# Optimization experiments

Hardware: AMD Instinct MI355X
Metric: run time of the kernel (lower is better)

## Reference

```python
import jax, jax.numpy as jnp
import numpy as np

N_HEAD = 16
HEAD_SIZE = 1024
EMBED = 1024
MULTI_HEAD_SIZE = HEAD_SIZE // N_HEAD  # 64; used only as the softmax scale (source bug)
B, S = 4, 2048


def setup_inputs() -> dict:
    key = jax.random.key(0)
    k1, k2, k3, k4 = jax.random.split(key, 4)
    x = jax.random.normal(k1, (B, S, EMBED), dtype=jnp.float32)
    w_qkv = jax.random.normal(k2, (3 * HEAD_SIZE, EMBED), dtype=jnp.float32) * 0.02
    w_proj = jax.random.normal(k3, (EMBED, HEAD_SIZE), dtype=jnp.float32) * 0.02
    b_proj = jax.random.normal(k4, (EMBED,), dtype=jnp.float32) * 0.02
    return {"x": x, "w_qkv": w_qkv, "w_proj": w_proj, "b_proj": b_proj}


def reference(x, w_qkv, w_proj, b_proj):
    # Fused QKV projection (Linear, no bias): [B,S,E] @ [E,3H] -> split
    qkv = jnp.einsum("bse,he->bsh", x, w_qkv)  # [B,S,3H]
    q, k, v = jnp.split(qkv, 3, axis=-1)       # each [B,S,H]
    # Source's non-flash path: attention over FULL Head_size dim (not per-head),
    # scaled by sqrt(multi_head_size) -- reproduced faithfully.
    scale = 1.0 / np.sqrt(MULTI_HEAD_SIZE).astype(np.float32)
    scores = jnp.einsum("bqh,bkh->bqk", q, k) * scale  # [B,S,S]
    probs = jax.nn.softmax(scores, axis=-1)            # dropout = identity (eval)
    out = jnp.einsum("bqk,bkh->bqh", probs, v)         # [B,S,H]
    # Faithful scrambling reshape: transpose(1,2).contiguous().view(B,S,H)
    Bn, Sn, H = out.shape
    out = jnp.swapaxes(out, 1, 2).reshape(Bn, Sn, H)
    # Output projection + residual dropout (identity in eval)
    out = jnp.einsum("bsh,eh->bse", out, w_proj) + b_proj
    return out
```

## Files before the change

### kernel.cpp

```cpp
#include <hip/hip_runtime.h>


typedef float f32x4 __attribute__((ext_vector_type(4)));
typedef short bf16x8 __attribute__((ext_vector_type(8)));
typedef short bf16x4 __attribute__((ext_vector_type(4)));
typedef unsigned short u16;

__device__ inline u16 f2bf(float f) {
  union { float f; unsigned u; } x; x.f = f;
  unsigned r = x.u + 0x7fffu + ((x.u >> 16) & 1u);
  return (u16)(r >> 16);
}

__device__ inline void gload_lds16(const void* g, void* l) {
  __builtin_amdgcn_global_load_lds(
      (const __attribute__((address_space(1))) void*)g,
      (__attribute__((address_space(3))) void*)l, 16, 0, 0);
}

__global__ __launch_bounds__(256) void cvt_kernel(const float* __restrict__ in,
                                                  u16* __restrict__ out, int n8) {
  int i = blockIdx.x * 256 + threadIdx.x;
  if (i >= n8) return;
  f32x4 a = *(const f32x4*)&in[(long)i * 8];
  f32x4 b = *(const f32x4*)&in[(long)i * 8 + 4];
  bf16x8 o;
#pragma unroll
  for (int j = 0; j < 4; ++j) { o[j] = (short)f2bf(a[j]); o[4 + j] = (short)f2bf(b[j]); }
  *(bf16x8*)&out[(long)i * 8] = o;
}

__global__ __launch_bounds__(256) void transpose_v(const u16* __restrict__ qkvb,
                                                   u16* __restrict__ vT) {
  __shared__ u16 tile[64][72];
  const int t = threadIdx.x;
  const long b = blockIdx.z;
  const int k0 = blockIdx.x * 64, h0 = blockIdx.y * 64;
  const u16* v = qkvb + b * 2048 * 3072 + 2048;
#pragma unroll
  for (int i = 0; i < 2; ++i) {
    int s = i * 256 + t; int r = s >> 3, c = (s & 7) * 8;
    bf16x8 val = *(const bf16x8*)&v[(long)(k0 + r) * 3072 + h0 + c];
    *(bf16x8*)&tile[r][c] = val;
  }
  __syncthreads();
  u16* o = vT + b * 1024 * 2048;
#pragma unroll
  for (int i = 0; i < 2; ++i) {
    int s = i * 256 + t; int r = s >> 3, c = (s & 7) * 8;
    bf16x8 val;
#pragma unroll
    for (int j = 0; j < 8; ++j) val[j] = tile[c + j][r];
    *(bf16x8*)&o[(long)(h0 + r) * 2048 + k0 + c] = val;
  }
}

__global__ __launch_bounds__(256) void softmax_k(const float* __restrict__ S,
                                                 u16* __restrict__ P,
                                                 long sS, long sP) {
  const int t = threadIdx.x;
  const float* row = S + (long)blockIdx.z * sS + (long)blockIdx.x * 2048;
  u16* prow = P + (long)blockIdx.z * sP + (long)blockIdx.x * 2048;
  f32x4 v0 = *(const f32x4*)&row[t * 8];
  f32x4 v1 = *(const f32x4*)&row[t * 8 + 4];
  float m = v0[0];
#pragma unroll
  for (int j = 1; j < 4; ++j) m = fmaxf(m, v0[j]);
#pragma unroll
  for (int j = 0; j < 4; ++j) m = fmaxf(m, v1[j]);
#pragma unroll
  for (int o = 32; o; o >>= 1) m = fmaxf(m, __shfl_xor(m, o));
  __shared__ float red[8];
  if ((t & 63) == 0) red[t >> 6] = m;
  __syncthreads();
  m = fmaxf(fmaxf(red[0], red[1]), fmaxf(red[2], red[3]));
  const float C = 0.18033688011112042f;
  float e[8], s = 0.f;
#pragma unroll
  for (int j = 0; j < 4; ++j) { e[j] = exp2f((v0[j] - m) * C); s += e[j]; }
#pragma unroll
  for (int j = 0; j < 4; ++j) { e[4 + j] = exp2f((v1[j] - m) * C); s += e[4 + j]; }
#pragma unroll
  for (int o = 32; o; o >>= 1) s += __shfl_xor(s, o);
  if ((t & 63) == 0) red[4 + (t >> 6)] = s;
  __syncthreads();
  float inv = 1.f / (red[4] + red[5] + red[6] + red[7]);
  bf16x8 ov;
#pragma unroll
  for (int j = 0; j < 8; ++j) ov[j] = (short)f2bf(e[j] * inv);
  *(bf16x8*)&prow[t * 8] = ov;
}

template <int MODE, int BMT>
__global__ __launch_bounds__(512, 2) void gemm8(const u16* __restrict__ A0, int lda, long sAz,
                                                const u16* __restrict__ B0, int ldb, long sBz,
                                                void* __restrict__ C0, int ldc, long sCz,
                                                const float* __restrict__ bias, int K) {
  constexpr int MF = BMT / 32;
  constexpr int LA = BMT / 128;
  extern __shared__ __align__(16) u16 smem[];
  u16* Ab = smem;
  u16* Bb = smem + 4 * BMT * 32;
  const int t = threadIdx.x, lane = t & 63, wv = t >> 6;
  const int wr = wv >> 2, wc = wv & 3;
  const int fr = lane & 15, hi = lane >> 4;
  const long row0 = (long)blockIdx.y * BMT, col0 = (long)blockIdx.x * 256;
  const u16* A = A0 + (long)blockIdx.z * sAz;
  const u16* B = B0 + (long)blockIdx.z * sBz;

  f32x4 acc[MF][4];
#pragma unroll
  for (int m = 0; m < MF; ++m)
#pragma unroll
    for (int n = 0; n < 4; ++n) acc[m][n] = (f32x4){0.f, 0.f, 0.f, 0.f};

  auto stageA = [&](int buf, int ks, int k0) {
#pragma unroll
    for (int i = 0; i < LA; ++i) {
      const int l2 = i * 512 + t;
      const int r = l2 >> 2, ck = l2 & 3;
      gload_lds16(A + (row0 + r) * (long)lda + k0 + ks * 32 + ck * 8,
                  Ab + (buf * 2 + ks) * BMT * 32 + (i * 512 + wv * 64) * 8);
    }
  };
  auto stageB = [&](int buf, int ks, int k0) {
#pragma unroll
    for (int i = 0; i < 2; ++i) {
      const int l2 = i * 512 + t;
      const int r = l2 >> 2, ck = l2 & 3;
      gload_lds16(B + (col0 + r) * (long)ldb + k0 + ks * 32 + ck * 8,
                  Bb + (buf * 2 + ks) * 256 * 32 + (i * 512 + wv * 64) * 8);
    }
  };

  bf16x8 bfr[4];
  auto loadB = [&](int buf, int ks) {
#pragma unroll
    for (int n = 0; n < 4; ++n)
      bfr[n] = *(const bf16x8*)(Bb + ((buf * 2 + ks) * 256 + wc * 64 + n * 16 + fr) * 32 + hi * 8);
  };
  auto phase = [&](int buf, int ks, int mlo) {
    bf16x8 afr[MF / 2];
#pragma unroll
    for (int m = 0; m < MF / 2; ++m)
      afr[m] = *(const bf16x8*)(Ab + ((buf * 2 + ks) * BMT + wr * (BMT / 2) + (mlo + m) * 16 + fr) * 32 + hi * 8);
    __builtin_amdgcn_s_setprio(1);
#pragma unroll
    for (int m = 0; m < MF / 2; ++m)
#pragma unroll
      for (int n = 0; n < 4; ++n)
        acc[mlo + m][n] = __builtin_amdgcn_mfma_f32_16x16x32_bf16(afr[m], bfr[n], acc[mlo + m][n], 0, 0, 0);
    __builtin_amdgcn_s_setprio(0);
  };

  stageA(0, 0, 0); stageB(0, 0, 0); stageA(0, 1, 0); stageB(0, 1, 0);
  __builtin_amdgcn_sched_barrier(0);
  asm volatile("s_waitcnt vmcnt(0)" ::: "memory");
  __builtin_amdgcn_s_barrier();
  __builtin_amdgcn_sched_barrier(0);

  const int NT = K >> 6;
  for (int kt = 0; kt < NT; ++kt) {
    const int c = kt & 1;
    const int kn = (kt + 1 < NT) ? ((kt + 1) << 6) : 0;
    stageA(c ^ 1, 0, kn); loadB(c, 0); phase(c, 0, 0);
    stageB(c ^ 1, 0, kn); phase(c, 0, MF / 2);
    __builtin_amdgcn_sched_barrier(0);
    if constexpr (LA == 2) asm volatile("s_waitcnt vmcnt(4)" ::: "memory");
    else                   asm volatile("s_waitcnt vmcnt(3)" ::: "memory");
    __builtin_amdgcn_s_barrier();
    __builtin_amdgcn_sched_barrier(0);
    stageA(c ^ 1, 1, kn); loadB(c, 1); phase(c, 1, 0);
    stageB(c ^ 1, 1, kn); phase(c, 1, MF / 2);
    __builtin_amdgcn_sched_barrier(0);
    if constexpr (LA == 2) asm volatile("s_waitcnt vmcnt(4)" ::: "memory");
    else                   asm volatile("s_waitcnt vmcnt(3)" ::: "memory");
    __builtin_amdgcn_s_barrier();
    __builtin_amdgcn_sched_barrier(0);
  }

#pragma unroll
  for (int m = 0; m < MF; ++m)
#pragma unroll
    for (int n = 0; n < 4; ++n) {
      const long r0 = row0 + wr * (BMT / 2) + m * 16 + hi * 4;
      const long c = col0 + wc * 64 + n * 16 + fr;
      if (MODE == 0) {
        float* C = (float*)C0 + (long)blockIdx.z * sCz;
#pragma unroll
        for (int j = 0; j < 4; ++j) C[(r0 + j) * ldc + c] = acc[m][n][j];
      } else if (MODE == 1) {
        u16* C = (u16*)C0 + (long)blockIdx.z * sCz;
#pragma unroll
        for (int j = 0; j < 4; ++j) C[(r0 + j) * ldc + c] = f2bf(acc[m][n][j]);
      } else if (MODE == 2) {
        u16* C = (u16*)C0 + (long)blockIdx.z * sCz;
        const int q0 = (int)r0;
        const long dr = 2 * c + (q0 >> 10);
        bf16x4 pk;
#pragma unroll
        for (int j = 0; j < 4; ++j) pk[j] = (short)f2bf(acc[m][n][j]);
        *(bf16x4*)&C[dr * 1024 + (q0 & 1023)] = pk;
      } else {
        float* C = (float*)C0 + (long)blockIdx.z * sCz;
        const float bv = bias[c];
#pragma unroll
        for (int j = 0; j < 4; ++j) C[(r0 + j) * ldc + c] = acc[m][n][j] + bv;
      }
    }
}

extern "C" void kernel_launch(void* const* d_in, const int* in_sizes, int n_in,
                              void* d_out, int out_size, void* d_ws, size_t ws_size,
                              hipStream_t stream) {
  const float* x      = (const float*)d_in[0];
  const float* w_qkv  = (const float*)d_in[1];
  const float* w_proj = (const float*)d_in[2];
  const float* b_proj = (const float*)d_in[3];
  float* out = (float*)d_out;
  char* ws = (char*)d_ws;

  u16*   xb     = (u16*)(ws + 0);
  u16*   wqkvb  = (u16*)(ws + 16777216);
  u16*   wprojb = (u16*)(ws + 23068672);
  u16*   qkvb   = (u16*)(ws + 25165824);
  u16*   vT     = (u16*)(ws + 75497472);
  u16*   out2   = (u16*)(ws + 92274688);
  float* scores = (float*)(ws + 109051904);
  const bool full = ws_size >= 209715200ull;
  u16* probs = (u16*)(ws + (full ? 176160768 : 125829120));

  const int LDS256 = (4 * 256 * 32 + 4 * 256 * 32) * 2;
  const int LDS128 = (4 * 128 * 32 + 4 * 256 * 32) * 2;
  hipFuncSetAttribute((const void*)gemm8<1, 128>, hipFuncAttributeMaxDynamicSharedMemorySize, LDS128);
  hipFuncSetAttribute((const void*)gemm8<0, 256>, hipFuncAttributeMaxDynamicSharedMemorySize, LDS256);
  hipFuncSetAttribute((const void*)gemm8<2, 128>, hipFuncAttributeMaxDynamicSharedMemorySize, LDS128);
  hipFuncSetAttribute((const void*)gemm8<3, 128>, hipFuncAttributeMaxDynamicSharedMemorySize, LDS128);

  cvt_kernel<<<4096, 256, 0, stream>>>(x, xb, 1048576);
  cvt_kernel<<<1536, 256, 0, stream>>>(w_qkv, wqkvb, 393216);
  cvt_kernel<<<512, 256, 0, stream>>>(w_proj, wprojb, 131072);

  gemm8<1, 128><<<dim3(12, 64, 1), 512, LDS128, stream>>>(xb, 1024, 0, wqkvb, 1024, 0,
                                                          qkvb, 3072, 0, nullptr, 1024);
  transpose_v<<<dim3(32, 16, 4), 256, 0, stream>>>(qkvb, vT);

  const long sQ = 2048L * 3072;
  if (full) {
    gemm8<0, 256><<<dim3(8, 8, 4), 512, LDS256, stream>>>(qkvb, 3072, sQ, qkvb + 1024, 3072, sQ,
                                                          scores, 2048, 2048L * 2048, nullptr, 1024);
    softmax_k<<<dim3(2048, 1, 4), 256, 0, stream>>>(scores, probs, 2048L * 2048, 2048L * 2048);
    gemm8<2, 128><<<dim3(4, 16, 4), 512, LDS128, stream>>>(probs, 2048, 2048L * 2048, vT, 2048, 2048L * 1024,
                                                           out2, 1024, 2048L * 1024, nullptr, 2048);
  } else {
    for (int b = 0; b < 4; ++b) {
      const u16* qb = qkvb + (long)b * sQ;
      gemm8<0, 256><<<dim3(8, 8, 1), 512, LDS256, stream>>>(qb, 3072, 0, qb + 1024, 3072, 0,
                                                            scores, 2048, 0, nullptr, 1024);
      softmax_k<<<dim3(2048, 1, 1), 256, 0, stream>>>(scores, probs, 0, 0);
      gemm8<2, 128><<<dim3(4, 16, 1), 512, LDS128, stream>>>(probs, 2048, 0, vT + (long)b * 2048 * 1024, 2048, 0,
                                                             out2 + (long)b * 2048 * 1024, 1024, 0, nullptr, 2048);
    }
  }

  gemm8<3, 128><<<dim3(4, 64, 1), 512, LDS128, stream>>>(out2, 1024, 0, wprojb, 1024, 0,
                                                         out, 1024, 0, b_proj, 1024);
}
```

Before: 299.2 us.

## Swizzle GEMM LDS layout, remap blocks across XCDs, restructure k-loop pipeline

The GEMM kernel now XOR-swizzles the 16-byte chunks within each LDS row, so fragment reads avoid bank conflicts. Block indices are remapped so that consecutive blocks are spread across the 8 XCDs in contiguous groups, aiming for better L2 locality. The k-loop is reorganised to wait and barrier first, load all A and B fragments, issue the next prefetch, and then run the MFMAs in two halves split by lgkmcnt waits. In exchange, fragment registers grow and the remapping adds integer division overhead.

```diff
diff --git a/kernel.cpp b/kernel.cpp
--- a/kernel.cpp
+++ b/kernel.cpp
@@ -91,110 +91,124 @@
   *(bf16x8*)&prow[t * 8] = ov;
 }
 
-template <int MODE, int BMT>
-__global__ __launch_bounds__(512, 2) void gemm8(const u16* __restrict__ A0, int lda, long sAz,
+template <int MODE, int BM>
+__global__ __launch_bounds__(512, 2) void gemm9(const u16* __restrict__ A0, int lda, long sAz,
                                                 const u16* __restrict__ B0, int ldb, long sBz,
                                                 void* __restrict__ C0, int ldc, long sCz,
                                                 const float* __restrict__ bias, int K) {
-  constexpr int MF = BMT / 32;
-  constexpr int LA = BMT / 128;
+  constexpr int MR = BM / 32;
+  constexpr int LA = BM / 128;
   extern __shared__ __align__(16) u16 smem[];
   u16* Ab = smem;
-  u16* Bb = smem + 4 * BMT * 32;
+  u16* Bb = smem + 4 * BM * 32;
   const int t = threadIdx.x, lane = t & 63, wv = t >> 6;
   const int wr = wv >> 2, wc = wv & 3;
   const int fr = lane & 15, hi = lane >> 4;
-  const long row0 = (long)blockIdx.y * BMT, col0 = (long)blockIdx.x * 256;
-  const u16* A = A0 + (long)blockIdx.z * sAz;
-  const u16* B = B0 + (long)blockIdx.z * sBz;
-
-  f32x4 acc[MF][4];
-#pragma unroll
-  for (int m = 0; m < MF; ++m)
+
+  const int gx = gridDim.x, gy = gridDim.y;
+  long L = ((long)blockIdx.z * gy + blockIdx.y) * gx + blockIdx.x;
+  const long NB = (long)gx * gy * gridDim.z;
+  if ((NB & 7) == 0) L = (L & 7) * (NB >> 3) + (L >> 3);
+  const int bx = (int)(L % gx);
+  const int by = (int)((L / gx) % gy);
+  const int bz = (int)(L / ((long)gx * gy));
+
+  const long row0 = (long)by * BM, col0 = (long)bx * 256;
+  const u16* A = A0 + (long)bz * sAz;
+  const u16* B = B0 + (long)bz * sBz;
+
+  f32x4 acc[MR][4];
+#pragma unroll
+  for (int m = 0; m < MR; ++m)
 #pragma unroll
     for (int n = 0; n < 4; ++n) acc[m][n] = (f32x4){0.f, 0.f, 0.f, 0.f};
 
-  auto stageA = [&](int buf, int ks, int k0) {
+  auto stA = [&](int buf, int ks, int k0) {
 #pragma unroll
     for (int i = 0; i < LA; ++i) {
-      const int l2 = i * 512 + t;
-      const int r = l2 >> 2, ck = l2 & 3;
-      gload_lds16(A + (row0 + r) * (long)lda + k0 + ks * 32 + ck * 8,
-                  Ab + (buf * 2 + ks) * BMT * 32 + (i * 512 + wv * 64) * 8);
-    }
-  };
-  auto stageB = [&](int buf, int ks, int k0) {
+      const int l = i * 512 + t;
+      const int r = l >> 2, sl = (l & 3) ^ (r & 3);
+      gload_lds16(A + (row0 + r) * (long)lda + k0 + ks * 32 + sl * 8,
+                  Ab + (buf * 2 + ks) * BM * 32 + (i * 512 + wv * 64) * 8);
+    }
+  };
+  auto stB = [&](int buf, int ks, int k0) {
 #pragma unroll
     for (int i = 0; i < 2; ++i) {
-      const int l2 = i * 512 + t;
-      const int r = l2 >> 2, ck = l2 & 3;
-      gload_lds16(B + (col0 + r) * (long)ldb + k0 + ks * 32 + ck * 8,
+      const int l = i * 512 + t;
+      const int r = l >> 2, sl = (l & 3) ^ (r & 3);
+      gload_lds16(B + (col0 + r) * (long)ldb + k0 + ks * 32 + sl * 8,
                   Bb + (buf * 2 + ks) * 256 * 32 + (i * 512 + wv * 64) * 8);
     }
   };
-
-  bf16x8 bfr[4];
-  auto loadB = [&](int buf, int ks) {
-#pragma unroll
-    for (int n = 0; n < 4; ++n)
-      bfr[n] = *(const bf16x8*)(Bb + ((buf * 2 + ks) * 256 + wc * 64 + n * 16 + fr) * 32 + hi * 8);
-  };
-  auto phase = [&](int buf, int ks, int mlo) {
-    bf16x8 afr[MF / 2];
-#pragma unroll
-    for (int m = 0; m < MF / 2; ++m)
-      afr[m] = *(const bf16x8*)(Ab + ((buf * 2 + ks) * BMT + wr * (BMT / 2) + (mlo + m) * 16 + fr) * 32 + hi * 8);
-    __builtin_amdgcn_s_setprio(1);
-#pragma unroll
-    for (int m = 0; m < MF / 2; ++m)
-#pragma unroll
-      for (int n = 0; n < 4; ++n)
-        acc[mlo + m][n] = __builtin_amdgcn_mfma_f32_16x16x32_bf16(afr[m], bfr[n], acc[mlo + m][n], 0, 0, 0);
-    __builtin_amdgcn_s_setprio(0);
-  };
-
-  stageA(0, 0, 0); stageB(0, 0, 0); stageA(0, 1, 0); stageB(0, 1, 0);
-  __builtin_amdgcn_sched_barrier(0);
-  asm volatile("s_waitcnt vmcnt(0)" ::: "memory");
-  __builtin_amdgcn_s_barrier();
-  __builtin_amdgcn_sched_barrier(0);
+  auto aAddr = [&](int buf, int ks, int m) -> const u16* {
+    const int r = wr * (BM / 2) + m * 16 + fr;
+    return Ab + ((buf * 2 + ks) * BM + r) * 32 + (hi ^ (fr & 3)) * 8;
+  };
+  auto bAddr = [&](int buf, int ks, int n) -> const u16* {
+    const int r = wc * 64 + n * 16 + fr;
+    return Bb + ((buf * 2 + ks) * 256 + r) * 32 + (hi ^ (fr & 3)) * 8;
+  };
+
+  stA(0, 0, 0); stB(0, 0, 0);
+  stA(0, 1, 0); stB(0, 1, 0);
 
   const int NT = K >> 6;
   for (int kt = 0; kt < NT; ++kt) {
-    const int c = kt & 1;
-    const int kn = (kt + 1 < NT) ? ((kt + 1) << 6) : 0;
-    stageA(c ^ 1, 0, kn); loadB(c, 0); phase(c, 0, 0);
-    stageB(c ^ 1, 0, kn); phase(c, 0, MF / 2);
-    __builtin_amdgcn_sched_barrier(0);
-    if constexpr (LA == 2) asm volatile("s_waitcnt vmcnt(4)" ::: "memory");
-    else                   asm volatile("s_waitcnt vmcnt(3)" ::: "memory");
-    __builtin_amdgcn_s_barrier();
-    __builtin_amdgcn_sched_barrier(0);
-    stageA(c ^ 1, 1, kn); loadB(c, 1); phase(c, 1, 0);
-    stageB(c ^ 1, 1, kn); phase(c, 1, MF / 2);
-    __builtin_amdgcn_sched_barrier(0);
-    if constexpr (LA == 2) asm volatile("s_waitcnt vmcnt(4)" ::: "memory");
-    else                   asm volatile("s_waitcnt vmcnt(3)" ::: "memory");
-    __builtin_amdgcn_s_barrier();
-    __builtin_amdgcn_sched_barrier(0);
-  }
-
-#pragma unroll
-  for (int m = 0; m < MF; ++m)
+    const int buf = kt & 1;
+    const int kn = (kt + 1) << 6;
+    const bool pf = (kt + 1 < NT);
+#pragma unroll
+    for (int ks = 0; ks < 2; ++ks) {
+      if constexpr (LA == 2) asm volatile("s_waitcnt vmcnt(4)" ::: "memory");
+      else                   asm volatile("s_waitcnt vmcnt(3)" ::: "memory");
+      __builtin_amdgcn_s_barrier();
+      __builtin_amdgcn_sched_barrier(0);
+      bf16x8 afr[MR], b01[2], b23[2];
+#pragma unroll
+      for (int m = 0; m < MR; ++m) afr[m] = *(const bf16x8*)aAddr(buf, ks, m);
+#pragma unroll
+      for (int n = 0; n < 2; ++n) b01[n] = *(const bf16x8*)bAddr(buf, ks, n);
+#pragma unroll
+      for (int n = 0; n < 2; ++n) b23[n] = *(const bf16x8*)bAddr(buf, ks, 2 + n);
+      if (pf) { stA(buf ^ 1, ks, kn); stB(buf ^ 1, ks, kn); }
+      asm volatile("s_waitcnt lgkmcnt(2)" ::: "memory");
+      __builtin_amdgcn_sched_barrier(0);
+      __builtin_amdgcn_s_setprio(1);
+#pragma unroll
+      for (int m = 0; m < MR; ++m) {
+        acc[m][0] = __builtin_amdgcn_mfma_f32_16x16x32_bf16(afr[m], b01[0], acc[m][0], 0, 0, 0);
+        acc[m][1] = __builtin_amdgcn_mfma_f32_16x16x32_bf16(afr[m], b01[1], acc[m][1], 0, 0, 0);
+      }
+      __builtin_amdgcn_s_setprio(0);
+      asm volatile("s_waitcnt lgkmcnt(0)" ::: "memory");
+      __builtin_amdgcn_sched_barrier(0);
+      __builtin_amdgcn_s_setprio(1);
+#pragma unroll
+      for (int m = 0; m < MR; ++m) {
+        acc[m][2] = __builtin_amdgcn_mfma_f32_16x16x32_bf16(afr[m], b23[0], acc[m][2], 0, 0, 0);
+        acc[m][3] = __builtin_amdgcn_mfma_f32_16x16x32_bf16(afr[m], b23[1], acc[m][3], 0, 0, 0);
+      }
+      __builtin_amdgcn_s_setprio(0);
+    }
+  }
+
+#pragma unroll
+  for (int m = 0; m < MR; ++m)
 #pragma unroll
     for (int n = 0; n < 4; ++n) {
-      const long r0 = row0 + wr * (BMT / 2) + m * 16 + hi * 4;
+      const long r0 = row0 + wr * (BM / 2) + m * 16 + hi * 4;
       const long c = col0 + wc * 64 + n * 16 + fr;
       if (MODE == 0) {
-        float* C = (float*)C0 + (long)blockIdx.z * sCz;
+        float* C = (float*)C0 + (long)bz * sCz;
 #pragma unroll
         for (int j = 0; j < 4; ++j) C[(r0 + j) * ldc + c] = acc[m][n][j];
       } else if (MODE == 1) {
-        u16* C = (u16*)C0 + (long)blockIdx.z * sCz;
+        u16* C = (u16*)C0 + (long)bz * sCz;
 #pragma unroll
         for (int j = 0; j < 4; ++j) C[(r0 + j) * ldc + c] = f2bf(acc[m][n][j]);
       } else if (MODE == 2) {
-        u16* C = (u16*)C0 + (long)blockIdx.z * sCz;
+        u16* C = (u16*)C0 + (long)bz * sCz;
         const int q0 = (int)r0;
         const long dr = 2 * c + (q0 >> 10);
         bf16x4 pk;
@@ -202,7 +216,7 @@
         for (int j = 0; j < 4; ++j) pk[j] = (short)f2bf(acc[m][n][j]);
         *(bf16x4*)&C[dr * 1024 + (q0 & 1023)] = pk;
       } else {
-        float* C = (float*)C0 + (long)blockIdx.z * sCz;
+        float* C = (float*)C0 + (long)bz * sCz;
         const float bv = bias[c];
 #pragma unroll
         for (int j = 0; j < 4; ++j) C[(r0 + j) * ldc + c] = acc[m][n][j] + bv;
@@ -230,39 +244,39 @@
   const bool full = ws_size >= 209715200ull;
   u16* probs = (u16*)(ws + (full ? 176160768 : 125829120));
 
+  const int LDS128 = (4 * 128 * 32 + 4 * 256 * 32) * 2;
   const int LDS256 = (4 * 256 * 32 + 4 * 256 * 32) * 2;
-  const int LDS128 = (4 * 128 * 32 + 4 * 256 * 32) * 2;
-  hipFuncSetAttribute((const void*)gemm8<1, 128>, hipFuncAttributeMaxDynamicSharedMemorySize, LDS128);
-  hipFuncSetAttribute((const void*)gemm8<0, 256>, hipFuncAttributeMaxDynamicSharedMemorySize, LDS256);
-  hipFuncSetAttribute((const void*)gemm8<2, 128>, hipFuncAttributeMaxDynamicSharedMemorySize, LDS128);
-  hipFuncSetAttribute((const void*)gemm8<3, 128>, hipFuncAttributeMaxDynamicSharedMemorySize, LDS128);
+  hipFuncSetAttribute((const void*)gemm9<1, 128>, hipFuncAttributeMaxDynamicSharedMemorySize, LDS128);
+  hipFuncSetAttribute((const void*)gemm9<0, 256>, hipFuncAttributeMaxDynamicSharedMemorySize, LDS256);
+  hipFuncSetAttribute((const void*)gemm9<2, 128>, hipFuncAttributeMaxDynamicSharedMemorySize, LDS128);
+  hipFuncSetAttribute((const void*)gemm9<3, 128>, hipFuncAttributeMaxDynamicSharedMemorySize, LDS128);
 
   cvt_kernel<<<4096, 256, 0, stream>>>(x, xb, 1048576);
   cvt_kernel<<<1536, 256, 0, stream>>>(w_qkv, wqkvb, 393216);
   cvt_kernel<<<512, 256, 0, stream>>>(w_proj, wprojb, 131072);
 
-  gemm8<1, 128><<<dim3(12, 64, 1), 512, LDS128, stream>>>(xb, 1024, 0, wqkvb, 1024, 0,
+  gemm9<1, 128><<<dim3(12, 64, 1), 512, LDS128, stream>>>(xb, 1024, 0, wqkvb, 1024, 0,
                                                           qkvb, 3072, 0, nullptr, 1024);
   transpose_v<<<dim3(32, 16, 4), 256, 0, stream>>>(qkvb, vT);
 
   const long sQ = 2048L * 3072;
   if (full) {
-    gemm8<0, 256><<<dim3(8, 8, 4), 512, LDS256, stream>>>(qkvb, 3072, sQ, qkvb + 1024, 3072, sQ,
+    gemm9<0, 256><<<dim3(8, 8, 4), 512, LDS256, stream>>>(qkvb, 3072, sQ, qkvb + 1024, 3072, sQ,
                                                           scores, 2048, 2048L * 2048, nullptr, 1024);
     softmax_k<<<dim3(2048, 1, 4), 256, 0, stream>>>(scores, probs, 2048L * 2048, 2048L * 2048);
-    gemm8<2, 128><<<dim3(4, 16, 4), 512, LDS128, stream>>>(probs, 2048, 2048L * 2048, vT, 2048, 2048L * 1024,
+    gemm9<2, 128><<<dim3(4, 16, 4), 512, LDS128, stream>>>(probs, 2048, 2048L * 2048, vT, 2048, 2048L * 1024,
                                                            out2, 1024, 2048L * 1024, nullptr, 2048);
   } else {
     for (int b = 0; b < 4; ++b) {
       const u16* qb = qkvb + (long)b * sQ;
-      gemm8<0, 256><<<dim3(8, 8, 1), 512, LDS256, stream>>>(qb, 3072, 0, qb + 1024, 3072, 0,
+      gemm9<0, 256><<<dim3(8, 8, 1), 512, LDS256, stream>>>(qb, 3072, 0, qb + 1024, 3072, 0,
                                                             scores, 2048, 0, nullptr, 1024);
       softmax_k<<<dim3(2048, 1, 1), 256, 0, stream>>>(scores, probs, 0, 0);
-      gemm8<2, 128><<<dim3(4, 16, 1), 512, LDS128, stream>>>(probs, 2048, 0, vT + (long)b * 2048 * 1024, 2048, 0,
+      gemm9<2, 128><<<dim3(4, 16, 1), 512, LDS128, stream>>>(probs, 2048, 0, vT + (long)b * 2048 * 1024, 2048, 0,
                                                              out2 + (long)b * 2048 * 1024, 1024, 0, nullptr, 2048);
     }
   }
 
-  gemm8<3, 128><<<dim3(4, 64, 1), 512, LDS128, stream>>>(out2, 1024, 0, wprojb, 1024, 0,
+  gemm9<3, 128><<<dim3(4, 64, 1), 512, LDS128, stream>>>(out2, 1024, 0, wprojb, 1024, 0,
                                                          out, 1024, 0, b_proj, 1024);
 }
```

Result: no change. 295.3 us (-1.3%).
